# Performance work log

Measured on AMD Instinct MI355X. Metric: run time of the kernel, lower is better.

## Reference

```python
import jax, jax.numpy as jnp
import numpy as np

B, V, F, NT, NR, R = 4096, 200, 4, 16, 5, 16
G = NT * NR  # 80
MAX_RHO = 12.0
NLIG = 7
EPS = 1e-5
TWO_PI = 2.0 * np.pi


def setup_inputs() -> dict:
    key = jax.random.key(0)
    ks = jax.random.split(key, 16)
    input_feat = jax.random.normal(ks[0], (B, V, F), dtype=jnp.float32)
    rho = jax.random.uniform(ks[1], (B, V, 1), dtype=jnp.float32) * MAX_RHO
    theta = jax.random.uniform(ks[2], (B, V, 1), dtype=jnp.float32) * TWO_PI
    mask = (jax.random.uniform(ks[3], (B, V, 1)) < 0.9).astype(jnp.float32)
    # gaussian centers on a polar grid (per input feature channel)
    rc = jnp.linspace(0.0, MAX_RHO, NR)
    tc = jnp.linspace(0.0, TWO_PI, NT, endpoint=False)
    mu_rho = jnp.broadcast_to(jnp.repeat(rc, NT), (F, G)) + 0.05 * jax.random.normal(ks[4], (F, G))
    mu_theta = jnp.broadcast_to(jnp.tile(tc, NR), (F, G)) + 0.05 * jax.random.normal(ks[5], (F, G))
    sigma_rho = jnp.full((F, G), MAX_RHO / 8.0, dtype=jnp.float32)
    sigma_theta = jnp.ones((F, G), dtype=jnp.float32)
    conv_W = jax.random.normal(ks[6], (F, G, G), dtype=jnp.float32) / np.sqrt(G)
    conv_b = jnp.zeros((F, G), dtype=jnp.float32)
    fc1_W = jax.random.normal(ks[7], (G, F * G), dtype=jnp.float32) / np.sqrt(F * G)
    fc1_b = jnp.zeros((G,), dtype=jnp.float32)
    fc2_W = jax.random.normal(ks[8], (64, G * G), dtype=jnp.float32) / np.sqrt(G * G)
    fc2_b = jnp.zeros((64,), dtype=jnp.float32)
    fco_W = jax.random.normal(ks[9], (NLIG, 64), dtype=jnp.float32) / 8.0
    fco_b = jnp.zeros((NLIG,), dtype=jnp.float32)
    return dict(input_feat=input_feat, rho=rho, theta=theta, mask=mask,
                mu_rho=mu_rho, mu_theta=mu_theta, sigma_rho=sigma_rho, sigma_theta=sigma_theta,
                conv_W=conv_W, conv_b=conv_b, fc1_W=fc1_W, fc1_b=fc1_b,
                fc2_W=fc2_W, fc2_b=fc2_b, fco_W=fco_W, fco_b=fco_b)


def reference(input_feat, rho, theta, mask, mu_rho, mu_theta, sigma_rho, sigma_theta,
              conv_W, conv_b, fc1_W, fc1_b, fc2_W, fc2_b, fco_W, fco_b):
    rot = (TWO_PI / R) * jnp.arange(R, dtype=jnp.float32)

    def conv_feat(x_f, mr, mt, sr, st, W, b):
        # x_f: [B,V,1]; mr/mt/sr/st: [G]; W: [G,G]; b: [G]
        @jax.checkpoint
        def step(carry, ang):
            th = jnp.mod(theta + ang, TWO_PI)                      # [B,V,1]
            g = jnp.exp(-(rho - mr) ** 2 / (sr ** 2 + EPS)
                        - (th - mt) ** 2 / (st ** 2 + EPS)) * mask  # [B,V,G]
            agg = jnp.einsum('bvg,bvo->bg', g, x_f)                 # [B,G]
            return carry, jax.nn.relu(agg @ W + b)
        _, outs = jax.lax.scan(step, None, rot)                      # [R,B,G]
        return outs.max(axis=0)                                      # [B,G]

    descs = [conv_feat(input_feat[:, :, i:i + 1], mu_rho[i], mu_theta[i],
                       sigma_rho[i], sigma_theta[i], conv_W[i], conv_b[i])
             for i in range(F)]
    x = jnp.stack(descs, axis=1).reshape(input_feat.shape[0], -1)   # [B, F*G]
    x = jax.nn.relu(x @ fc1_W.T + fc1_b)                             # [B, G]
    gram = (x.T @ x / x.shape[0]).reshape(1, -1)                     # [1, G*G]
    # dropout is identity at inference
    h = jax.nn.relu(gram @ fc2_W.T + fc2_b)                          # [1, 64]
    return h @ fco_W.T + fco_b                                       # [1, NLIG]
```

## Files before the change

kernel.cpp:

```cpp
#include <hip/hip_runtime.h>
#include <hip/hip_bf16.h>

#define BB 4096
#define VV 200
#define FF 4
#define GG 80
#define RR 16
#define NLIG 7
#define PVMAX 216
#define TWO_PI_F 6.2831853071795864769f
#define ANG_STEP 0.39269908169872414f
#define INV_ANG_STEP 2.5464790894703255f
#define LOG2E_F 1.4426950408889634f

typedef float v2f __attribute__((ext_vector_type(2)));

__device__ __forceinline__ float fexp2(float x) {
#if __has_builtin(__builtin_amdgcn_exp2f)
    return __builtin_amdgcn_exp2f(x);
#else
    return exp2f(x);
#endif
}

__device__ __forceinline__ v2f pk_fma(v2f a, v2f b, v2f c) {
    v2f d;
    asm("v_pk_fma_f32 %0, %1, %2, %3" : "=v"(d) : "v"(a), "v"(b), "v"(c));
    return d;
}
__device__ __forceinline__ v2f pk_mul(v2f a, v2f b) {
    v2f d;
    asm("v_pk_mul_f32 %0, %1, %2" : "=v"(d) : "v"(a), "v"(b));
    return d;
}

template<int C>
__device__ __forceinline__ void chain(const v2f (&Kp)[8], v2f (&aggE)[8],
                                      v2f (&aggO)[8], float M, float B) {
    const float B2 = B * B;
    v2f u;  u.x = M;  u.y = M * B;
    v2f w2; w2.x = B2; w2.y = B2;
    #pragma unroll
    for (int i = 0; i < 8; ++i) {
        const int idx = ((2 * i + 16 - C) & 15) >> 1;
        if constexpr ((C & 1) == 0) aggE[idx] = pk_fma(u, Kp[i], aggE[idx]);
        else                        aggO[idx] = pk_fma(u, Kp[i], aggO[idx]);
        if (i < 7) u = pk_mul(u, w2);
    }
}

#define OFF_PV_RA 0
#define OFF_PV_VB 1728
#define OFF_PV_X  3456
#define OFF_CNTW  6912
#define OFF_PS    7232
#define OFF_SSIG  7300
#define OFF_AGGL  0
#define OFF_DESC  20480
#define OFF_HP    21760
#define UNI_SIZE  23104

__global__ __launch_bounds__(320, 6) void masif_main(
    const float* __restrict__ xin,
    const float* __restrict__ rho,
    const float* __restrict__ theta,
    const float* __restrict__ mask,
    const float* __restrict__ mu_rho,
    const float* __restrict__ mu_theta,
    const float* __restrict__ sigma_rho,
    const float* __restrict__ sigma_theta,
    const float* __restrict__ conv_W,
    const float* __restrict__ conv_b,
    const float* __restrict__ fc1_W,
    const float* __restrict__ fc1_b,
    float* __restrict__ xbuf)
{
    const int b = blockIdx.x;
    const int t = threadIdx.x;
    const int f = t / GG;
    const int g = t % GG;
    const int lane = t & 63;
    const int w = t >> 6;

    __shared__ __align__(16) char U[UNI_SIZE];
    float2* pv_ra = reinterpret_cast<float2*>(U + OFF_PV_RA);
    float2* pv_vb = reinterpret_cast<float2*>(U + OFF_PV_VB);
    float (*pv_x)[PVMAX] = reinterpret_cast<float(*)[PVMAX]>(U + OFF_PV_X);
    int (*cntw)[RR] = reinterpret_cast<int(*)[RR]>(U + OFF_CNTW);
    int* ps = reinterpret_cast<int*>(U + OFF_PS);
    float* ssig = reinterpret_cast<float*>(U + OFF_SSIG);
    float (*aggL)[RR][GG] = reinterpret_cast<float(*)[RR][GG]>(U + OFF_AGGL);
    float* desc_s = reinterpret_cast<float*>(U + OFF_DESC);
    float* hp_s = reinterpret_cast<float*>(U + OFF_HP);

    const float mr  = mu_rho[f * GG + g];
    const float mt  = mu_theta[f * GG + g];
    const float sr  = sigma_rho[f * GG + g];
    const float st  = sigma_theta[f * GG + g];
    const float nisr2 = -LOG2E_F / (sr * sr + 1e-5f);
    const float nist2 = -LOG2E_F / (st * st + 1e-5f);
    const float c1 = 2.0f * ANG_STEP * nist2;

    float rh = 0.f, a0 = 0.f, mx0 = 0.f, mx1 = 0.f, mx2 = 0.f, mx3 = 0.f;
    int j0 = 0;
    bool keep = false;
    if (t < VV) {
        const int idx = b * VV + t;
        const float th = theta[idx];
        const float m  = mask[idx];
        keep = (m != 0.0f);
        rh = rho[idx];
        j0 = (int)(th * INV_ANG_STEP);
        if (j0 > RR - 1) j0 = RR - 1;
        a0 = fmaf(-(float)j0, ANG_STEP, th);
        const float4 xv = *reinterpret_cast<const float4*>(&xin[idx * 4]);
        mx0 = m * xv.x; mx1 = m * xv.y; mx2 = m * xv.z; mx3 = m * xv.w;
    }
    if (t == 0) { ssig[0] = nisr2; ssig[1] = nist2; }

    v2f Kp[8];
    #pragma unroll
    for (int i = 0; i < 8; ++i) {
        const float m0 = (float)(2 * i), m1 = (float)(2 * i + 1);
        Kp[i].x = fexp2(nist2 * (ANG_STEP * ANG_STEP) * m0 * m0);
        Kp[i].y = fexp2(nist2 * (ANG_STEP * ANG_STEP) * m1 * m1);
    }

    int rank = 0, cnt_lane = 0;
    #pragma unroll
    for (int c = 0; c < RR; ++c) {
        const unsigned long long mbl = __ballot(keep && (j0 == c));
        if (keep && (j0 == c))
            rank = (int)__popcll(mbl & ((1ull << lane) - 1ull));
        if (lane == c) cnt_lane = (int)__popcll(mbl);
    }
    if (lane < RR) cntw[w][lane] = cnt_lane;
    __syncthreads();

    const float s_nisr2 = ssig[0], s_nist2 = ssig[1];
    const int myflag = (__float_as_int(nisr2) == __float_as_int(s_nisr2)) &&
                       (__float_as_int(nist2) == __float_as_int(s_nist2));
    float va = 0.f, Bv = 0.f;
    if (t < VV) {
        const float s_c1 = 2.0f * ANG_STEP * s_nist2;
        va = fmaf(a0 * a0, s_nist2, (rh * rh) * s_nisr2);
        Bv = fexp2(s_c1 * a0);
    }
    if (t == 0) {
        int s = 0;
        #pragma unroll
        for (int c = 0; c < RR; ++c) {
            ps[c] = s;
            const int cc = cntw[0][c] + cntw[1][c] + cntw[2][c]
                         + cntw[3][c] + cntw[4][c];
            s += (cc + 1) & ~1;
        }
        ps[RR] = s;
    }
    if (t < PVMAX) {
        pv_ra[t] = make_float2(0.f, 0.f);
        pv_vb[t] = make_float2(0.f, 0.f);
        pv_x[0][t] = 0.f; pv_x[1][t] = 0.f; pv_x[2][t] = 0.f; pv_x[3][t] = 0.f;
    }
    const int uniOK = __syncthreads_and(myflag);

    if (keep) {
        int off = 0;
        #pragma unroll
        for (int w2 = 0; w2 < 4; ++w2)
            if (w2 < w) off += cntw[w2][j0];
        const int pos = ps[j0] + off + rank;
        pv_ra[pos] = make_float2(rh, a0);
        pv_vb[pos] = make_float2(va, Bv);
        pv_x[0][pos] = mx0; pv_x[1][pos] = mx1;
        pv_x[2][pos] = mx2; pv_x[3][pos] = mx3;
    }
    __syncthreads();

    v2f aggE[8], aggO[8];
    #pragma unroll
    for (int i = 0; i < 8; ++i) {
        aggE[i].x = 0.f; aggE[i].y = 0.f;
        aggO[i].x = 0.f; aggO[i].y = 0.f;
    }

    if (uniOK) {
        const float ct1 = -2.0f * nist2 * mt;
        const float ct2 = -2.0f * nisr2 * mr;
        const float Cc  = fmaf(mt * mt, nist2, (mr * mr) * nisr2);
        const float Bt  = fexp2(-c1 * mt);
        int sprev = 0;
#define CLSF(C) { \
        const int send = __builtin_amdgcn_readfirstlane(ps[(C) + 1]); \
        for (int v = sprev; v < send; v += 2) { \
            const float4 ra2 = *reinterpret_cast<const float4*>(&pv_ra[v]); \
            const float4 vb2 = *reinterpret_cast<const float4*>(&pv_vb[v]); \
            const v2f s2 = *reinterpret_cast<const v2f*>(&pv_x[f][v]); \
            const float tA = fmaf(ra2.y, ct1, fmaf(ra2.x, ct2, vb2.x + Cc)); \
            const float MsA = fexp2(tA) * s2.x; \
            const float BA = vb2.y * Bt; \
            const float tB = fmaf(ra2.w, ct1, fmaf(ra2.z, ct2, vb2.z + Cc)); \
            const float MsB = fexp2(tB) * s2.y; \
            const float BBv = vb2.w * Bt; \
            chain<(C)>(Kp, aggE, aggO, MsA, BA); \
            chain<(C)>(Kp, aggE, aggO, MsB, BBv); \
        } \
        sprev = send; }
        CLSF(0)  CLSF(1)  CLSF(2)  CLSF(3)
        CLSF(4)  CLSF(5)  CLSF(6)  CLSF(7)
        CLSF(8)  CLSF(9)  CLSF(10) CLSF(11)
        CLSF(12) CLSF(13) CLSF(14) CLSF(15)
#undef CLSF
    } else {
        int sprev = 0;
#define CLSS(C) { \
        const int send = __builtin_amdgcn_readfirstlane(ps[(C) + 1]); \
        for (int v = sprev; v < send; v += 2) { \
            const float4 ra2 = *reinterpret_cast<const float4*>(&pv_ra[v]); \
            const v2f s2 = *reinterpret_cast<const v2f*>(&pv_x[f][v]); \
            const float drA = ra2.x - mr, xA = ra2.y - mt; \
            const float arA = (drA * drA) * nisr2; \
            const float MA = fexp2(fmaf(xA * xA, nist2, arA)) * s2.x; \
            const float BA = fexp2(xA * c1); \
            const float drB = ra2.z - mr, xB = ra2.w - mt; \
            const float arB = (drB * drB) * nisr2; \
            const float MB = fexp2(fmaf(xB * xB, nist2, arB)) * s2.y; \
            const float BBv = fexp2(xB * c1); \
            chain<(C)>(Kp, aggE, aggO, MA, BA); \
            chain<(C)>(Kp, aggE, aggO, MB, BBv); \
        } \
        sprev = send; }
        CLSS(0)  CLSS(1)  CLSS(2)  CLSS(3)
        CLSS(4)  CLSS(5)  CLSS(6)  CLSS(7)
        CLSS(8)  CLSS(9)  CLSS(10) CLSS(11)
        CLSS(12) CLSS(13) CLSS(14) CLSS(15)
#undef CLSS
    }
    __syncthreads();

    #pragma unroll
    for (int k = 0; k < 8; ++k) {
        aggL[f][2 * k][g]     = aggE[k].x + aggO[(k + 7) & 7].y;
        aggL[f][2 * k + 1][g] = aggE[k].y + aggO[k].x;
    }
    __syncthreads();

    v2f racc2[RR];
    {
        const float cb = conv_b[f * GG + g];
        #pragma unroll
        for (int r = 0; r < RR; ++r) { racc2[r].x = cb; racc2[r].y = 0.f; }
    }
    for (int g4 = 0; g4 < GG; g4 += 4) {
        const float* wp = &conv_W[(f * GG + g4) * GG + g];
        v2f wA, wB;
        wA.x = wp[0];      wA.y = wp[GG];
        wB.x = wp[2 * GG]; wB.y = wp[3 * GG];
        #pragma unroll
        for (int r = 0; r < RR; ++r) {
            const float4 a4 = *reinterpret_cast<const float4*>(&aggL[f][r][g4]);
            v2f aA, aB;
            aA.x = a4.x; aA.y = a4.y;
            aB.x = a4.z; aB.y = a4.w;
            racc2[r] = pk_fma(aA, wA, racc2[r]);
            racc2[r] = pk_fma(aB, wB, racc2[r]);
        }
    }
    float mxr = racc2[0].x + racc2[0].y;
    #pragma unroll
    for (int r = 1; r < RR; ++r) mxr = fmaxf(mxr, racc2[r].x + racc2[r].y);
    desc_s[f * GG + g] = fmaxf(mxr, 0.0f);

    __syncthreads();

    {
        const v2f* wrow = reinterpret_cast<const v2f*>(&fc1_W[g * (FF * GG) + f * GG]);
        const v2f* drow = reinterpret_cast<const v2f*>(&desc_s[f * GG]);
        v2f a2; a2.x = 0.f; a2.y = 0.f;
        #pragma unroll 4
        for (int k = 0; k < GG / 2; ++k) a2 = pk_fma(drow[k], wrow[k], a2);
        hp_s[f * GG + g] = a2.x + a2.y;
    }
    __syncthreads();
    if (t < GG) {
        const float a1 = ((hp_s[t] + hp_s[GG + t]) + (hp_s[2 * GG + t] + hp_s[3 * GG + t]))
                         + fc1_b[t];
        xbuf[b * GG + t] = fmaxf(a1, 0.0f);
    }
}

__global__ __launch_bounds__(256) void gram_partial(
    const float* __restrict__ xbuf,
    float* __restrict__ gpart)
{
    const int blk = blockIdx.x;
    const int t = threadIdx.x;
    __shared__ float xs[64][GG];

    for (int i = t; i < 64 * GG; i += 256) {
        int bb = i / GG, jj = i % GG;
        xs[bb][jj] = xbuf[(blk * 64 + bb) * GG + jj];
    }
    __syncthreads();

    const int ti = t / 16, tj = t % 16;
    float acc[5][5];
    #pragma unroll
    for (int u = 0; u < 5; ++u)
        #pragma unroll
        for (int w = 0; w < 5; ++w) acc[u][w] = 0.0f;

    for (int bb = 0; bb < 64; ++bb) {
        float xi[5], xj[5];
        #pragma unroll
        for (int u = 0; u < 5; ++u) { xi[u] = xs[bb][ti * 5 + u]; xj[u] = xs[bb][tj * 5 + u]; }
        #pragma unroll
        for (int u = 0; u < 5; ++u)
            #pragma unroll
            for (int w = 0; w < 5; ++w)
                acc[u][w] = fmaf(xi[u], xj[w], acc[u][w]);
    }

    #pragma unroll
    for (int u = 0; u < 5; ++u)
        #pragma unroll
        for (int w = 0; w < 5; ++w)
            gpart[blk * (GG * GG) + (ti * 5 + u) * GG + (tj * 5 + w)] = acc[u][w];
}

__global__ __launch_bounds__(128) void head_partial(
    const float* __restrict__ gpart,
    const float* __restrict__ fc2_W,
    float* __restrict__ hpp)
{
    const int p = blockIdx.x;
    const int t = threadIdx.x;
    __shared__ float gs[100];

    if (t < 100) {
        const int k = p * 100 + t;
        float s = 0.f;
        #pragma unroll 8
        for (int q = 0; q < 64; ++q) s += gpart[q * (GG * GG) + k];
        gs[t] = s * (1.0f / 4096.0f);
    }
    __syncthreads();
    if (t < 64) {
        const float* w = &fc2_W[t * (GG * GG) + p * 100];
        float a = 0.f;
        #pragma unroll 4
        for (int k = 0; k < 100; ++k) a = fmaf(gs[k], w[k], a);
        hpp[p * 64 + t] = a;
    }
}

__global__ __launch_bounds__(256) void head_final(
    const float* __restrict__ hpp,
    const float* __restrict__ fc2_b,
    const float* __restrict__ fco_W,
    const float* __restrict__ fco_b,
    float* __restrict__ out)
{
    const int t = threadIdx.x;
    const int part = t >> 6, j = t & 63;
    __shared__ float hq[4][64];
    __shared__ float hs[64];
    float a = 0.f;
    #pragma unroll 4
    for (int p = part * 16; p < part * 16 + 16; ++p) a += hpp[p * 64 + j];
    hq[part][j] = a;
    __syncthreads();
    if (t < 64)
        hs[t] = fmaxf(((hq[0][t] + hq[1][t]) + (hq[2][t] + hq[3][t])) + fc2_b[t], 0.0f);
    __syncthreads();
    if (t < NLIG) {
        float o = fco_b[t];
        #pragma unroll
        for (int jj = 0; jj < 64; ++jj) o = fmaf(hs[jj], fco_W[t * 64 + jj], o);
        out[t] = o;
    }
}

extern "C" void kernel_launch(void* const* d_in, const int* in_sizes, int n_in,
                              void* d_out, int out_size, void* d_ws, size_t ws_size,
                              hipStream_t stream) {
    const float* input_feat  = (const float*)d_in[0];
    const float* rho         = (const float*)d_in[1];
    const float* theta       = (const float*)d_in[2];
    const float* mask        = (const float*)d_in[3];
    const float* mu_rho      = (const float*)d_in[4];
    const float* mu_theta    = (const float*)d_in[5];
    const float* sigma_rho   = (const float*)d_in[6];
    const float* sigma_theta = (const float*)d_in[7];
    const float* conv_W      = (const float*)d_in[8];
    const float* conv_b      = (const float*)d_in[9];
    const float* fc1_W       = (const float*)d_in[10];
    const float* fc1_b       = (const float*)d_in[11];
    const float* fc2_W       = (const float*)d_in[12];
    const float* fc2_b       = (const float*)d_in[13];
    const float* fco_W       = (const float*)d_in[14];
    const float* fco_b       = (const float*)d_in[15];

    float* xbuf  = (float*)d_ws;
    float* gpart = (float*)((char*)d_ws + (size_t)BB * GG * 4);
    float* hpp   = (float*)((char*)d_ws + (size_t)BB * GG * 4
                                        + (size_t)64 * GG * GG * 4);

    masif_main<<<BB, 320, 0, stream>>>(input_feat, rho, theta, mask,
                                       mu_rho, mu_theta, sigma_rho, sigma_theta,
                                       conv_W, conv_b, fc1_W, fc1_b, xbuf);
    gram_partial<<<64, 256, 0, stream>>>(xbuf, gpart);
    head_partial<<<64, 128, 0, stream>>>(gpart, fc2_W, hpp);
    head_final<<<1, 256, 0, stream>>>(hpp, fc2_b, fco_W, fco_b, (float*)d_out);
}
```

Before: 322.2 us.

## Remap threads so each wave shares a rho ring and skip out-of-range vertex pairs

Threads are remapped so each wavefront covers 16 gaussians from one radial ring across all 4 features. A wave-uniform test then skips vertex pairs whose radial distance makes the gaussian weight fall below 2^-26. Per-vertex data moves from interleaved float2 arrays to separate scalar arrays, so the rho value can be loaded alone before the cull test. The angular math is done with packed FP32 ops. The skip adds a ballot and a branch to every pair, and drops only negligible terms, so results change slightly.

```diff
diff --git a/kernel.cpp b/kernel.cpp
--- a/kernel.cpp
+++ b/kernel.cpp
@@ -12,6 +12,7 @@
 #define ANG_STEP 0.39269908169872414f
 #define INV_ANG_STEP 2.5464790894703255f
 #define LOG2E_F 1.4426950408889634f
+#define EXPCUT 26.0f
 
 typedef float v2f __attribute__((ext_vector_type(2)));
 
@@ -33,6 +34,12 @@
     asm("v_pk_mul_f32 %0, %1, %2" : "=v"(d) : "v"(a), "v"(b));
     return d;
 }
+__device__ __forceinline__ v2f pk_add(v2f a, v2f b) {
+    v2f d;
+    asm("v_pk_add_f32 %0, %1, %2" : "=v"(d) : "v"(a), "v"(b));
+    return d;
+}
+__device__ __forceinline__ v2f bc2(float x) { v2f r; r.x = x; r.y = x; return r; }
 
 template<int C>
 __device__ __forceinline__ void chain(const v2f (&Kp)[8], v2f (&aggE)[8],
@@ -49,8 +56,10 @@
     }
 }
 
-#define OFF_PV_RA 0
-#define OFF_PV_VB 1728
+#define OFF_RHO   0
+#define OFF_A0    864
+#define OFF_VA    1728
+#define OFF_BV    2592
 #define OFF_PV_X  3456
 #define OFF_CNTW  6912
 #define OFF_PS    7232
@@ -77,14 +86,18 @@
 {
     const int b = blockIdx.x;
     const int t = threadIdx.x;
+    const int lane = t & 63;
+    const int w = t >> 6;
+    const int fb = lane >> 4;
+    const int gb = w * 16 + (lane & 15);
     const int f = t / GG;
     const int g = t % GG;
-    const int lane = t & 63;
-    const int w = t >> 6;
 
     __shared__ __align__(16) char U[UNI_SIZE];
-    float2* pv_ra = reinterpret_cast<float2*>(U + OFF_PV_RA);
-    float2* pv_vb = reinterpret_cast<float2*>(U + OFF_PV_VB);
+    float* pv_rho = reinterpret_cast<float*>(U + OFF_RHO);
+    float* pv_a0  = reinterpret_cast<float*>(U + OFF_A0);
+    float* pv_va  = reinterpret_cast<float*>(U + OFF_VA);
+    float* pv_bv  = reinterpret_cast<float*>(U + OFF_BV);
     float (*pv_x)[PVMAX] = reinterpret_cast<float(*)[PVMAX]>(U + OFF_PV_X);
     int (*cntw)[RR] = reinterpret_cast<int(*)[RR]>(U + OFF_CNTW);
     int* ps = reinterpret_cast<int*>(U + OFF_PS);
@@ -93,10 +106,11 @@
     float* desc_s = reinterpret_cast<float*>(U + OFF_DESC);
     float* hp_s = reinterpret_cast<float*>(U + OFF_HP);
 
-    const float mr  = mu_rho[f * GG + g];
-    const float mt  = mu_theta[f * GG + g];
-    const float sr  = sigma_rho[f * GG + g];
-    const float st  = sigma_theta[f * GG + g];
+    const int pidx = fb * GG + gb;
+    const float mr  = mu_rho[pidx];
+    const float mt  = mu_theta[pidx];
+    const float sr  = sigma_rho[pidx];
+    const float st  = sigma_theta[pidx];
     const float nisr2 = -LOG2E_F / (sr * sr + 1e-5f);
     const float nist2 = -LOG2E_F / (st * st + 1e-5f);
     const float c1 = 2.0f * ANG_STEP * nist2;
@@ -158,8 +172,7 @@
         ps[RR] = s;
     }
     if (t < PVMAX) {
-        pv_ra[t] = make_float2(0.f, 0.f);
-        pv_vb[t] = make_float2(0.f, 0.f);
+        pv_rho[t] = 0.f; pv_a0[t] = 0.f; pv_va[t] = 0.f; pv_bv[t] = 0.f;
         pv_x[0][t] = 0.f; pv_x[1][t] = 0.f; pv_x[2][t] = 0.f; pv_x[3][t] = 0.f;
     }
     const int uniOK = __syncthreads_and(myflag);
@@ -170,8 +183,7 @@
         for (int w2 = 0; w2 < 4; ++w2)
             if (w2 < w) off += cntw[w2][j0];
         const int pos = ps[j0] + off + rank;
-        pv_ra[pos] = make_float2(rh, a0);
-        pv_vb[pos] = make_float2(va, Bv);
+        pv_rho[pos] = rh; pv_a0[pos] = a0; pv_va[pos] = va; pv_bv[pos] = Bv;
         pv_x[0][pos] = mx0; pv_x[1][pos] = mx1;
         pv_x[2][pos] = mx2; pv_x[3][pos] = mx3;
     }
@@ -189,21 +201,28 @@
         const float ct2 = -2.0f * nisr2 * mr;
         const float Cc  = fmaf(mt * mt, nist2, (mr * mr) * nisr2);
         const float Bt  = fexp2(-c1 * mt);
+        const v2f ct1_2 = bc2(ct1), ct2_2 = bc2(ct2), Cc2 = bc2(Cc), Bt2 = bc2(Bt);
+        const float R2cut = EXPCUT / (-s_nisr2);
         int sprev = 0;
 #define CLSF(C) { \
         const int send = __builtin_amdgcn_readfirstlane(ps[(C) + 1]); \
         for (int v = sprev; v < send; v += 2) { \
-            const float4 ra2 = *reinterpret_cast<const float4*>(&pv_ra[v]); \
-            const float4 vb2 = *reinterpret_cast<const float4*>(&pv_vb[v]); \
-            const v2f s2 = *reinterpret_cast<const v2f*>(&pv_x[f][v]); \
-            const float tA = fmaf(ra2.y, ct1, fmaf(ra2.x, ct2, vb2.x + Cc)); \
-            const float MsA = fexp2(tA) * s2.x; \
-            const float BA = vb2.y * Bt; \
-            const float tB = fmaf(ra2.w, ct1, fmaf(ra2.z, ct2, vb2.z + Cc)); \
-            const float MsB = fexp2(tB) * s2.y; \
-            const float BBv = vb2.w * Bt; \
-            chain<(C)>(Kp, aggE, aggO, MsA, BA); \
-            chain<(C)>(Kp, aggE, aggO, MsB, BBv); \
+            const v2f rho2 = *reinterpret_cast<const v2f*>(&pv_rho[v]); \
+            const float dA = rho2.x - mr, dB = rho2.y - mr; \
+            const int okA = __any(dA * dA <= R2cut); \
+            const int okB = __any(dB * dB <= R2cut); \
+            if (okA | okB) { \
+                const v2f a02 = *reinterpret_cast<const v2f*>(&pv_a0[v]); \
+                const v2f va2 = *reinterpret_cast<const v2f*>(&pv_va[v]); \
+                const v2f bv2 = *reinterpret_cast<const v2f*>(&pv_bv[v]); \
+                const v2f s2  = *reinterpret_cast<const v2f*>(&pv_x[fb][v]); \
+                const v2f tt = pk_fma(a02, ct1_2, pk_fma(rho2, ct2_2, pk_add(va2, Cc2))); \
+                const v2f Bab = pk_mul(bv2, Bt2); \
+                const float MsA = fexp2(tt.x) * s2.x; \
+                const float MsB = fexp2(tt.y) * s2.y; \
+                if (okA) chain<(C)>(Kp, aggE, aggO, MsA, Bab.x); \
+                if (okB) chain<(C)>(Kp, aggE, aggO, MsB, Bab.y); \
+            } \
         } \
         sprev = send; }
         CLSF(0)  CLSF(1)  CLSF(2)  CLSF(3)
@@ -216,13 +235,14 @@
 #define CLSS(C) { \
         const int send = __builtin_amdgcn_readfirstlane(ps[(C) + 1]); \
         for (int v = sprev; v < send; v += 2) { \
-            const float4 ra2 = *reinterpret_cast<const float4*>(&pv_ra[v]); \
-            const v2f s2 = *reinterpret_cast<const v2f*>(&pv_x[f][v]); \
-            const float drA = ra2.x - mr, xA = ra2.y - mt; \
+            const v2f rho2 = *reinterpret_cast<const v2f*>(&pv_rho[v]); \
+            const v2f a02  = *reinterpret_cast<const v2f*>(&pv_a0[v]); \
+            const v2f s2   = *reinterpret_cast<const v2f*>(&pv_x[fb][v]); \
+            const float drA = rho2.x - mr, xA = a02.x - mt; \
             const float arA = (drA * drA) * nisr2; \
             const float MA = fexp2(fmaf(xA * xA, nist2, arA)) * s2.x; \
             const float BA = fexp2(xA * c1); \
-            const float drB = ra2.z - mr, xB = ra2.w - mt; \
+            const float drB = rho2.y - mr, xB = a02.y - mt; \
             const float arB = (drB * drB) * nisr2; \
             const float MB = fexp2(fmaf(xB * xB, nist2, arB)) * s2.y; \
             const float BBv = fexp2(xB * c1); \
@@ -240,8 +260,8 @@
 
     #pragma unroll
     for (int k = 0; k < 8; ++k) {
-        aggL[f][2 * k][g]     = aggE[k].x + aggO[(k + 7) & 7].y;
-        aggL[f][2 * k + 1][g] = aggE[k].y + aggO[k].x;
+        aggL[fb][2 * k][gb]     = aggE[k].x + aggO[(k + 7) & 7].y;
+        aggL[fb][2 * k + 1][gb] = aggE[k].y + aggO[k].x;
     }
     __syncthreads();
 
```

Measured after the change: 287.2 us, median of 2. -10.9%, faster.
